# Optimization experiments

Measured on AMD Instinct MI355X. Metric: run time of the kernel, lower is better.

## Reference

```python
import jax, jax.numpy as jnp
import numpy as np

N_NODE = 50000
N_EDGE = 625000
FDIM = 128
HID = 128
EPS = 1e-5


def setup_inputs() -> dict:
    key = jax.random.key(0)
    ks = jax.random.split(key, 12)
    node_feature = jax.random.normal(ks[0], (N_NODE, FDIM), dtype=jnp.float32)
    edge_matrix = jax.random.randint(ks[1], (2, N_EDGE), 0, N_NODE, dtype=jnp.int32)
    edge_feature = jax.random.normal(ks[2], (N_EDGE, FDIM), dtype=jnp.float32)
    in_dim = FDIM + FDIM  # concat(node, aggregated edge)
    s1 = 1.0 / np.sqrt(in_dim)
    s2 = 1.0 / np.sqrt(HID)
    W1 = jax.random.uniform(ks[3], (in_dim, HID), jnp.float32, -s1, s1)
    b1 = jax.random.uniform(ks[4], (HID,), jnp.float32, -s1, s1)
    W2 = jax.random.uniform(ks[5], (HID, HID), jnp.float32, -s2, s2)
    b2 = jax.random.uniform(ks[6], (HID,), jnp.float32, -s2, s2)
    W3 = jax.random.uniform(ks[7], (HID, FDIM), jnp.float32, -s2, s2)
    b3 = jax.random.uniform(ks[8], (FDIM,), jnp.float32, -s2, s2)
    gamma = jnp.ones((FDIM,), jnp.float32)
    beta = jnp.zeros((FDIM,), jnp.float32)
    return {"node_feature": node_feature, "edge_matrix": edge_matrix,
            "edge_feature": edge_feature, "W1": W1, "b1": b1, "W2": W2,
            "b2": b2, "W3": W3, "b3": b3, "gamma": gamma, "beta": beta}


def reference(node_feature, edge_matrix, edge_feature, W1, b1, W2, b2, W3, b3, gamma, beta):
    # receiver_idx = edge_matrix.T[:, 1] with edge_matrix [2, N_edge] -> row 1
    receiver_idx = edge_matrix[1]
    # scatter_add over receiver: [N_node, fdim]
    agg = jax.ops.segment_sum(edge_feature, receiver_idx, num_segments=node_feature.shape[0])
    x = jnp.concatenate([node_feature, agg], axis=-1)  # [N_node, 2*fdim]
    h = jax.nn.relu(x @ W1 + b1)
    h = jax.nn.relu(h @ W2 + b2)
    h = h @ W3 + b3
    # LayerNorm over last dim (eps = 1e-5, torch default)
    mu = jnp.mean(h, axis=-1, keepdims=True)
    var = jnp.mean((h - mu) ** 2, axis=-1, keepdims=True)
    h = (h - mu) * jax.lax.rsqrt(var + EPS) * gamma + beta
    return h + node_feature
```

## Files before the change

kernel.cpp:

```cpp
#include <hip/hip_runtime.h>
#include <hip/hip_bf16.h>

#define N_NODE 50000
#define N_EDGE 625000
#define FDIM 128
#define NB_SCAN 196

typedef __bf16 bf16x8 __attribute__((ext_vector_type(8)));
typedef float floatx4 __attribute__((ext_vector_type(4)));

#define MT 64
#define XS_LD 264
#define H_LD 136

__device__ inline bf16x8 as_bf16x8(uint4 v) {
    union { uint4 u; bf16x8 b; } c; c.u = v; return c.b;
}

__global__ __launch_bounds__(256) void hist_kernel(
    const int* __restrict__ recv, int* __restrict__ count, int* __restrict__ pos)
{
    int e = blockIdx.x * 256 + threadIdx.x;
    if (e < N_EDGE) pos[e] = atomicAdd(&count[recv[e]], 1);
}

__global__ __launch_bounds__(256) void scan1_kernel(
    const int* __restrict__ count, int* __restrict__ off, int* __restrict__ bsum)
{
    __shared__ int s[256];
    int t = threadIdx.x;
    int i = blockIdx.x * 256 + t;
    int v = (i < N_NODE) ? count[i] : 0;
    s[t] = v;
    __syncthreads();
    for (int d = 1; d < 256; d <<= 1) {
        int x = (t >= d) ? s[t - d] : 0;
        __syncthreads();
        s[t] += x;
        __syncthreads();
    }
    if (i < N_NODE) off[i] = s[t] - v;
    if (t == 255) bsum[blockIdx.x] = s[255];
}

__global__ __launch_bounds__(256) void scan2_kernel(
    int* __restrict__ off, const int* __restrict__ bsum)
{
    __shared__ int s[256];
    int t = threadIdx.x;
    int v = (t < NB_SCAN) ? bsum[t] : 0;
    s[t] = v;
    __syncthreads();
    for (int d = 1; d < 256; d <<= 1) {
        int x = (t >= d) ? s[t - d] : 0;
        __syncthreads();
        s[t] += x;
        __syncthreads();
    }
    int i = blockIdx.x * 256 + t;
    if (i < N_NODE) off[i] += s[blockIdx.x] - ((blockIdx.x < NB_SCAN) ? bsum[blockIdx.x] : 0);
    if (i == N_NODE) off[i] = N_EDGE;
}

__global__ __launch_bounds__(256) void fill_kernel(
    const int* __restrict__ recv, const int* __restrict__ pos,
    const int* __restrict__ off, int* __restrict__ eid)
{
    int e = blockIdx.x * 256 + threadIdx.x;
    if (e < N_EDGE) {
        int r = recv[e];
        eid[off[r] + pos[e]] = e;
    }
}

__global__ __launch_bounds__(256) void wrepack_kernel(
    const float* __restrict__ W1, const float* __restrict__ W2,
    const float* __restrict__ W3, uint4* __restrict__ wp)
{
    int g = blockIdx.x * 256 + threadIdx.x;
    int lane = g & 63;
    int nt = (g >> 6) & 7;
    int tile = g >> 9;
    const float* W; int k0;
    if (tile < 8)       { W = W1; k0 = tile * 32; }
    else if (tile < 12) { W = W2; k0 = (tile - 8) * 32; }
    else                { W = W3; k0 = (tile - 12) * 32; }
    int n = nt * 16 + (lane & 15);
    int kb = k0 + (lane >> 4) * 8;
    union { __bf16 b[8]; uint4 u; } p;
#pragma unroll
    for (int j = 0; j < 8; ++j) p.b[j] = (__bf16)W[(kb + j) * 128 + n];
    wp[g] = p.u;
}

__global__ __launch_bounds__(256) void gather_kernel(
    const float4* __restrict__ ef4, const int* __restrict__ off,
    const int* __restrict__ eid, uint2* __restrict__ agg)
{
    int wave = threadIdx.x >> 6;
    int lane = threadIdx.x & 63;
    int node = blockIdx.x * 4 + wave;
    int half = lane >> 5;
    int c = lane & 31;
    float4 acc = {0.f, 0.f, 0.f, 0.f};
    int s0 = off[node], e0 = off[node + 1];
    for (int base = s0; base < e0; base += 64) {
        int cnt = e0 - base; if (cnt > 64) cnt = 64;
        int ids = (lane < cnt) ? eid[base + lane] : 0;
        int j = 0;
        for (; j + 8 <= cnt; j += 8) {
            int ea = __shfl(ids, j + half);
            int eb = __shfl(ids, j + 2 + half);
            int ec = __shfl(ids, j + 4 + half);
            int ed = __shfl(ids, j + 6 + half);
            float4 va = ef4[(long)ea * 32 + c];
            float4 vb = ef4[(long)eb * 32 + c];
            float4 vc = ef4[(long)ec * 32 + c];
            float4 vd = ef4[(long)ed * 32 + c];
            acc.x += va.x + vb.x + vc.x + vd.x;
            acc.y += va.y + vb.y + vc.y + vd.y;
            acc.z += va.z + vb.z + vc.z + vd.z;
            acc.w += va.w + vb.w + vc.w + vd.w;
        }
        for (; j < cnt; j += 2) {
            if (j + half < cnt) {
                int e = __shfl(ids, j + half);
                float4 v = ef4[(long)e * 32 + c];
                acc.x += v.x; acc.y += v.y; acc.z += v.z; acc.w += v.w;
            }
        }
    }
    acc.x += __shfl_xor(acc.x, 32);
    acc.y += __shfl_xor(acc.y, 32);
    acc.z += __shfl_xor(acc.z, 32);
    acc.w += __shfl_xor(acc.w, 32);
    if (half == 0) {
        union { __bf16 b[4]; uint2 u; } p;
        p.b[0] = (__bf16)acc.x; p.b[1] = (__bf16)acc.y;
        p.b[2] = (__bf16)acc.z; p.b[3] = (__bf16)acc.w;
        agg[(long)node * 32 + c] = p.u;
    }
}

__global__ __launch_bounds__(256, 3) void mlp_kernel(
    const float* __restrict__ nodef, const int* __restrict__ agg32,
    const uint4* __restrict__ wp,
    const float* __restrict__ b1, const float* __restrict__ b2,
    const float* __restrict__ b3,
    const float* __restrict__ gamma, const float* __restrict__ beta,
    float* __restrict__ out)
{
    __shared__ __bf16 xs[MT * XS_LD];
    __shared__ __bf16 h1[MT * H_LD];
    __bf16* h2 = xs;

    const int t = threadIdx.x;
    const int wave = t >> 6;
    const int lane = t & 63;
    const int quad = lane >> 4;
    const int l16 = lane & 15;
    const int w16 = wave << 4;
    const int q8 = quad << 3;
    const int node0 = blockIdx.x * MT;

    const float4* nf4 = (const float4*)nodef;
#pragma unroll
    for (int i = 0; i < 8; ++i) {
        int it = i * 256 + t;
        int row = it >> 5;
        int c4 = it & 31;
        int node = node0 + row;
        if (node >= N_NODE) node = N_NODE - 1;
        float4 v = nf4[(long)node * 32 + c4];
        union { __bf16 b[4]; short4 s; } u;
        u.b[0] = (__bf16)v.x; u.b[1] = (__bf16)v.y;
        u.b[2] = (__bf16)v.z; u.b[3] = (__bf16)v.w;
        *(short4*)&xs[row * XS_LD + c4 * 4] = u.s;
    }
    const int4* ag4 = (const int4*)agg32;
#pragma unroll
    for (int i = 0; i < 4; ++i) {
        int it = i * 256 + t;
        int row = it >> 4;
        int c8 = it & 15;
        int node = node0 + row;
        if (node >= N_NODE) node = N_NODE - 1;
        int4 v = ag4[(long)node * 16 + c8];
        *(int4*)&xs[row * XS_LD + 128 + c8 * 8] = v;
    }

    floatx4 acc[8];
    const floatx4 zero = {0.f, 0.f, 0.f, 0.f};

    auto run_gemm = [&](const __bf16* A, int ldA, const uint4* __restrict__ wpt, int nk) {
#pragma unroll
        for (int nt = 0; nt < 8; ++nt) acc[nt] = zero;
        const __bf16* arow = A + (w16 + l16) * ldA + q8;
        bf16x8 a = *(const bf16x8*)arow;
        bf16x8 b[8];
#pragma unroll
        for (int nt = 0; nt < 8; ++nt) b[nt] = as_bf16x8(wpt[nt * 64 + lane]);
        for (int kc = 0; kc < nk; ++kc) {
            bf16x8 a2; bf16x8 b2[8];
            if (kc + 1 < nk) {
                a2 = *(const bf16x8*)(arow + (kc + 1) * 32);
#pragma unroll
                for (int nt = 0; nt < 8; ++nt)
                    b2[nt] = as_bf16x8(wpt[((kc + 1) * 8 + nt) * 64 + lane]);
            }
#pragma unroll
            for (int nt = 0; nt < 8; ++nt)
                acc[nt] = __builtin_amdgcn_mfma_f32_16x16x32_bf16(a, b[nt], acc[nt], 0, 0, 0);
            a = a2;
#pragma unroll
            for (int nt = 0; nt < 8; ++nt) b[nt] = b2[nt];
        }
    };

    auto epilogue_relu = [&](const float* __restrict__ bias, __bf16* H) {
#pragma unroll
        for (int nt = 0; nt < 8; ++nt) {
            int col = nt * 16 + l16;
            float bv = bias[col];
#pragma unroll
            for (int r = 0; r < 4; ++r) {
                float v = acc[nt][r] + bv;
                v = v > 0.f ? v : 0.f;
                H[(w16 + quad * 4 + r) * H_LD + col] = (__bf16)v;
            }
        }
    };

    __syncthreads();
    run_gemm(xs, XS_LD, wp, 8);
    epilogue_relu(b1, h1);
    __syncthreads();
    run_gemm(h1, H_LD, wp + 8 * 8 * 64, 4);
    epilogue_relu(b2, h2);
    __syncthreads();
    run_gemm(h2, H_LD, wp + 12 * 8 * 64, 4);

    float vout[8][4];
    float sum[4] = {0.f, 0.f, 0.f, 0.f};
    float sq[4]  = {0.f, 0.f, 0.f, 0.f};
#pragma unroll
    for (int nt = 0; nt < 8; ++nt) {
        int col = nt * 16 + l16;
        float bv = b3[col];
#pragma unroll
        for (int r = 0; r < 4; ++r) {
            float v = acc[nt][r] + bv;
            vout[nt][r] = v;
            sum[r] += v;
            sq[r] += v * v;
        }
    }
#pragma unroll
    for (int r = 0; r < 4; ++r) {
#pragma unroll
        for (int offs = 1; offs < 16; offs <<= 1) {
            sum[r] += __shfl_xor(sum[r], offs);
            sq[r]  += __shfl_xor(sq[r], offs);
        }
    }
    float mu[4], rs[4];
#pragma unroll
    for (int r = 0; r < 4; ++r) {
        mu[r] = sum[r] * (1.f / 128.f);
        float var = sq[r] * (1.f / 128.f) - mu[r] * mu[r];
        rs[r] = rsqrtf(var + 1e-5f);
    }
#pragma unroll
    for (int nt = 0; nt < 8; ++nt) {
        int col = nt * 16 + l16;
        float g = gamma[col], be = beta[col];
#pragma unroll
        for (int r = 0; r < 4; ++r) {
            int row = w16 + quad * 4 + r;
            int node = node0 + row;
            if (node < N_NODE) {
                long o = (long)node * 128 + col;
                out[o] = (vout[nt][r] - mu[r]) * rs[r] * g + be + nodef[o];
            }
        }
    }
}

extern "C" void kernel_launch(void* const* d_in, const int* in_sizes, int n_in,
                              void* d_out, int out_size, void* d_ws, size_t ws_size,
                              hipStream_t stream)
{
    const float* nodef = (const float*)d_in[0];
    const int*   em    = (const int*)d_in[1];
    const float* ef    = (const float*)d_in[2];
    const float* W1    = (const float*)d_in[3];
    const float* b1    = (const float*)d_in[4];
    const float* W2    = (const float*)d_in[5];
    const float* b2    = (const float*)d_in[6];
    const float* W3    = (const float*)d_in[7];
    const float* b3    = (const float*)d_in[8];
    const float* gamma = (const float*)d_in[9];
    const float* beta  = (const float*)d_in[10];
    float* out = (float*)d_out;

    int* count = (int*)d_ws;
    int* pos   = count + 50048;
    int* off   = pos + 625024;
    int* bsum  = off + 50048;
    int* eid   = bsum + 256;
    int* agg32 = eid + 625024;
    uint4* wp  = (uint4*)(agg32 + 3200000);

    const int* recv = em + N_EDGE;

    hipMemsetAsync(count, 0, (size_t)N_NODE * sizeof(int), stream);

    wrepack_kernel<<<32, 256, 0, stream>>>(W1, W2, W3, wp);

    int eblocks = (N_EDGE + 255) / 256;
    hist_kernel<<<eblocks, 256, 0, stream>>>(recv, count, pos);
    scan1_kernel<<<NB_SCAN, 256, 0, stream>>>(count, off, bsum);
    scan2_kernel<<<NB_SCAN, 256, 0, stream>>>(off, bsum);
    fill_kernel<<<eblocks, 256, 0, stream>>>(recv, pos, off, eid);
    gather_kernel<<<N_NODE / 4, 256, 0, stream>>>((const float4*)ef, off, eid, (uint2*)agg32);

    int mblocks = (N_NODE + MT - 1) / MT;
    mlp_kernel<<<mblocks, 256, 0, stream>>>(nodef, agg32, wp, b1, b2, b3,
                                            gamma, beta, out);
}
```

Baseline: 548.0 us.

## Merge memset into weight repack, use atomic slot fill, deepen GEMM prefetch

The memset of the count array moves into the weight-repack kernel, which removes one launch. The per-edge pos array is dropped: fill now takes its slots with atomics on a copied offset array. The gather tail loop is unrolled into fixed 4/2/1-pair steps, and the MLP GEMM prefetch grows from one to two k-chunks ahead. In exchange, edge order within a node becomes nondeterministic, the atomics in fill may contend, and the deeper prefetch raises register pressure under launch_bounds(256,3).

```diff
diff --git a/kernel.cpp b/kernel.cpp
--- a/kernel.cpp
+++ b/kernel.cpp
@@ -17,66 +17,16 @@
     union { uint4 u; bf16x8 b; } c; c.u = v; return c.b;
 }
 
-__global__ __launch_bounds__(256) void hist_kernel(
-    const int* __restrict__ recv, int* __restrict__ count, int* __restrict__ pos)
-{
-    int e = blockIdx.x * 256 + threadIdx.x;
-    if (e < N_EDGE) pos[e] = atomicAdd(&count[recv[e]], 1);
-}
-
-__global__ __launch_bounds__(256) void scan1_kernel(
-    const int* __restrict__ count, int* __restrict__ off, int* __restrict__ bsum)
-{
-    __shared__ int s[256];
-    int t = threadIdx.x;
-    int i = blockIdx.x * 256 + t;
-    int v = (i < N_NODE) ? count[i] : 0;
-    s[t] = v;
-    __syncthreads();
-    for (int d = 1; d < 256; d <<= 1) {
-        int x = (t >= d) ? s[t - d] : 0;
-        __syncthreads();
-        s[t] += x;
-        __syncthreads();
-    }
-    if (i < N_NODE) off[i] = s[t] - v;
-    if (t == 255) bsum[blockIdx.x] = s[255];
-}
-
-__global__ __launch_bounds__(256) void scan2_kernel(
-    int* __restrict__ off, const int* __restrict__ bsum)
-{
-    __shared__ int s[256];
-    int t = threadIdx.x;
-    int v = (t < NB_SCAN) ? bsum[t] : 0;
-    s[t] = v;
-    __syncthreads();
-    for (int d = 1; d < 256; d <<= 1) {
-        int x = (t >= d) ? s[t - d] : 0;
-        __syncthreads();
-        s[t] += x;
-        __syncthreads();
-    }
-    int i = blockIdx.x * 256 + t;
-    if (i < N_NODE) off[i] += s[blockIdx.x] - ((blockIdx.x < NB_SCAN) ? bsum[blockIdx.x] : 0);
-    if (i == N_NODE) off[i] = N_EDGE;
-}
-
-__global__ __launch_bounds__(256) void fill_kernel(
-    const int* __restrict__ recv, const int* __restrict__ pos,
-    const int* __restrict__ off, int* __restrict__ eid)
-{
-    int e = blockIdx.x * 256 + threadIdx.x;
-    if (e < N_EDGE) {
-        int r = recv[e];
-        eid[off[r] + pos[e]] = e;
-    }
-}
-
-__global__ __launch_bounds__(256) void wrepack_kernel(
+__global__ __launch_bounds__(256) void prep_kernel(
     const float* __restrict__ W1, const float* __restrict__ W2,
-    const float* __restrict__ W3, uint4* __restrict__ wp)
-{
+    const float* __restrict__ W3, uint4* __restrict__ wp,
+    int* __restrict__ count)
+{
+    if (blockIdx.x >= 32) {
+        int idx = (blockIdx.x - 32) * 256 + threadIdx.x;
+        for (int i = idx; i < N_NODE; i += 8192) count[i] = 0;
+        return;
+    }
     int g = blockIdx.x * 256 + threadIdx.x;
     int lane = g & 63;
     int nt = (g >> 6) & 7;
@@ -91,6 +41,66 @@
 #pragma unroll
     for (int j = 0; j < 8; ++j) p.b[j] = (__bf16)W[(kb + j) * 128 + n];
     wp[g] = p.u;
+}
+
+__global__ __launch_bounds__(256) void hist_kernel(
+    const int* __restrict__ recv, int* __restrict__ count)
+{
+    int e = blockIdx.x * 256 + threadIdx.x;
+    if (e < N_EDGE) atomicAdd(&count[recv[e]], 1);
+}
+
+__global__ __launch_bounds__(256) void scan1_kernel(
+    const int* __restrict__ count, int* __restrict__ off, int* __restrict__ bsum)
+{
+    __shared__ int s[256];
+    int t = threadIdx.x;
+    int i = blockIdx.x * 256 + t;
+    int v = (i < N_NODE) ? count[i] : 0;
+    s[t] = v;
+    __syncthreads();
+    for (int d = 1; d < 256; d <<= 1) {
+        int x = (t >= d) ? s[t - d] : 0;
+        __syncthreads();
+        s[t] += x;
+        __syncthreads();
+    }
+    if (i < N_NODE) off[i] = s[t] - v;
+    if (t == 255) bsum[blockIdx.x] = s[255];
+}
+
+__global__ __launch_bounds__(256) void scan2_kernel(
+    int* __restrict__ off, int* __restrict__ off2, const int* __restrict__ bsum)
+{
+    __shared__ int s[256];
+    int t = threadIdx.x;
+    int v = (t < NB_SCAN) ? bsum[t] : 0;
+    s[t] = v;
+    __syncthreads();
+    for (int d = 1; d < 256; d <<= 1) {
+        int x = (t >= d) ? s[t - d] : 0;
+        __syncthreads();
+        s[t] += x;
+        __syncthreads();
+    }
+    int i = blockIdx.x * 256 + t;
+    if (i < N_NODE) {
+        int o = off[i] + s[blockIdx.x] - ((blockIdx.x < NB_SCAN) ? bsum[blockIdx.x] : 0);
+        off[i] = o;
+        off2[i] = o;
+    }
+    if (i == N_NODE) off[i] = N_EDGE;
+}
+
+__global__ __launch_bounds__(256) void fill_kernel(
+    const int* __restrict__ recv, int* __restrict__ off2, int* __restrict__ eid)
+{
+    int e = blockIdx.x * 256 + threadIdx.x;
+    if (e < N_EDGE) {
+        int r = recv[e];
+        int slot = atomicAdd(&off2[r], 1);
+        eid[slot] = e;
+    }
 }
 
 __global__ __launch_bounds__(256) void gather_kernel(
@@ -122,12 +132,25 @@
             acc.z += va.z + vb.z + vc.z + vd.z;
             acc.w += va.w + vb.w + vc.w + vd.w;
         }
-        for (; j < cnt; j += 2) {
-            if (j + half < cnt) {
-                int e = __shfl(ids, j + half);
-                float4 v = ef4[(long)e * 32 + c];
-                acc.x += v.x; acc.y += v.y; acc.z += v.z; acc.w += v.w;
-            }
+        if (j + 4 <= cnt) {
+            int ea = __shfl(ids, j + half);
+            int eb = __shfl(ids, j + 2 + half);
+            float4 va = ef4[(long)ea * 32 + c];
+            float4 vb = ef4[(long)eb * 32 + c];
+            acc.x += va.x + vb.x; acc.y += va.y + vb.y;
+            acc.z += va.z + vb.z; acc.w += va.w + vb.w;
+            j += 4;
+        }
+        if (j + 2 <= cnt) {
+            int ea = __shfl(ids, j + half);
+            float4 va = ef4[(long)ea * 32 + c];
+            acc.x += va.x; acc.y += va.y; acc.z += va.z; acc.w += va.w;
+            j += 2;
+        }
+        if (j + half < cnt) {
+            int ea = __shfl(ids, j + half);
+            float4 va = ef4[(long)ea * 32 + c];
+            acc.x += va.x; acc.y += va.y; acc.z += va.z; acc.w += va.w;
         }
     }
     acc.x += __shfl_xor(acc.x, 32);
@@ -196,24 +219,31 @@
 #pragma unroll
         for (int nt = 0; nt < 8; ++nt) acc[nt] = zero;
         const __bf16* arow = A + (w16 + l16) * ldA + q8;
-        bf16x8 a = *(const bf16x8*)arow;
-        bf16x8 b[8];
-#pragma unroll
-        for (int nt = 0; nt < 8; ++nt) b[nt] = as_bf16x8(wpt[nt * 64 + lane]);
+        bf16x8 a0 = *(const bf16x8*)arow;
+        bf16x8 b0[8], b1v[8];
+#pragma unroll
+        for (int nt = 0; nt < 8; ++nt) b0[nt] = as_bf16x8(wpt[nt * 64 + lane]);
+        bf16x8 a1;
+        if (nk > 1) {
+            a1 = *(const bf16x8*)(arow + 32);
+#pragma unroll
+            for (int nt = 0; nt < 8; ++nt) b1v[nt] = as_bf16x8(wpt[(8 + nt) * 64 + lane]);
+        }
+#pragma unroll 8
         for (int kc = 0; kc < nk; ++kc) {
-            bf16x8 a2; bf16x8 b2[8];
-            if (kc + 1 < nk) {
-                a2 = *(const bf16x8*)(arow + (kc + 1) * 32);
+            bf16x8 a2; bf16x8 b2v[8];
+            if (kc + 2 < nk) {
+                a2 = *(const bf16x8*)(arow + (kc + 2) * 32);
 #pragma unroll
                 for (int nt = 0; nt < 8; ++nt)
-                    b2[nt] = as_bf16x8(wpt[((kc + 1) * 8 + nt) * 64 + lane]);
+                    b2v[nt] = as_bf16x8(wpt[((kc + 2) * 8 + nt) * 64 + lane]);
             }
 #pragma unroll
             for (int nt = 0; nt < 8; ++nt)
-                acc[nt] = __builtin_amdgcn_mfma_f32_16x16x32_bf16(a, b[nt], acc[nt], 0, 0, 0);
-            a = a2;
-#pragma unroll
-            for (int nt = 0; nt < 8; ++nt) b[nt] = b2[nt];
+                acc[nt] = __builtin_amdgcn_mfma_f32_16x16x32_bf16(a0, b0[nt], acc[nt], 0, 0, 0);
+            a0 = a1; a1 = a2;
+#pragma unroll
+            for (int nt = 0; nt < 8; ++nt) { b0[nt] = b1v[nt]; b1v[nt] = b2v[nt]; }
         }
     };
 
@@ -304,24 +334,22 @@
     float* out = (float*)d_out;
 
     int* count = (int*)d_ws;
-    int* pos   = count + 50048;
-    int* off   = pos + 625024;
-    int* bsum  = off + 50048;
+    int* off   = count + 50048;
+    int* off2  = off + 50048;
+    int* bsum  = off2 + 50048;
     int* eid   = bsum + 256;
     int* agg32 = eid + 625024;
     uint4* wp  = (uint4*)(agg32 + 3200000);
 
     const int* recv = em + N_EDGE;
 
-    hipMemsetAsync(count, 0, (size_t)N_NODE * sizeof(int), stream);
-
-    wrepack_kernel<<<32, 256, 0, stream>>>(W1, W2, W3, wp);
+    prep_kernel<<<64, 256, 0, stream>>>(W1, W2, W3, wp, count);
 
     int eblocks = (N_EDGE + 255) / 256;
-    hist_kernel<<<eblocks, 256, 0, stream>>>(recv, count, pos);
+    hist_kernel<<<eblocks, 256, 0, stream>>>(recv, count);
     scan1_kernel<<<NB_SCAN, 256, 0, stream>>>(count, off, bsum);
-    scan2_kernel<<<NB_SCAN, 256, 0, stream>>>(off, bsum);
-    fill_kernel<<<eblocks, 256, 0, stream>>>(recv, pos, off, eid);
+    scan2_kernel<<<NB_SCAN, 256, 0, stream>>>(off, off2, bsum);
+    fill_kernel<<<eblocks, 256, 0, stream>>>(recv, off2, eid);
     gather_kernel<<<N_NODE / 4, 256, 0, stream>>>((const float4*)ef, off, eid, (uint2*)agg32);
 
     int mblocks = (N_NODE + MT - 1) / MT;
```

Result: slower. 564.8 us (+3.1%).
